# Kernel optimization log

Measured on AMD Instinct MI355X. Metric: run time of the kernel, lower is better.

The kernel has to match this reference:

```python
import jax, jax.numpy as jnp
import numpy as np

TOP_K = 2

def setup_inputs() -> dict:
    key = jax.random.key(0)
    k1, k2, k3, k4 = jax.random.split(key, 4)
    B, S, H, E, F = 2, 1024, 1024, 16, 1024
    hidden_states = jax.random.normal(k1, (B, S, H), dtype=jnp.float32)
    router_w = jax.random.normal(k2, (H, E), dtype=jnp.float32) * 0.02
    w_gate_up = jax.random.normal(k3, (E, H, 2 * F), dtype=jnp.float32) * 0.02
    w_down = jax.random.normal(k4, (E, F, H), dtype=jnp.float32) * 0.02
    return {"hidden_states": hidden_states, "router_w": router_w,
            "w_gate_up": w_gate_up, "w_down": w_down}

def reference(hidden_states, router_w, w_gate_up, w_down):
    B, S, H = hidden_states.shape
    E = router_w.shape[-1]
    flat = hidden_states.reshape(-1, H)                      # [T, H]
    T = flat.shape[0]
    # Routing: topk_then_softmax (default softmax_order)
    logits = flat @ router_w                                 # [T, E]
    top_vals, top_idx = jax.lax.top_k(logits, TOP_K)         # [T, K]
    routing_weights = jax.nn.softmax(top_vals, axis=-1)      # [T, K]
    # Scatter routing weights into a dense combine matrix [T, E]
    combine = jnp.zeros((T, E), dtype=flat.dtype)
    combine = combine.at[jnp.arange(T)[:, None], top_idx].add(routing_weights)
    # Fused expert FFN (per _FusedExpertTemplate, act_fn = SiLU-gated)
    gu = jnp.einsum('th,ehf->etf', flat, w_gate_up)          # [E, T, 2F]
    gate, up = jnp.split(gu, 2, axis=-1)
    gated = jax.nn.silu(gate) * up                           # [E, T, F]
    expert_out = jnp.einsum('etf,efh->eth', gated, w_down)   # [E, T, H]
    out = jnp.einsum('eth,te->th', expert_out, combine)      # [T, H]
    return out.reshape(B, S, H)
```

## Files before the change

kernel.cpp:

```cpp
#include <hip/hip_runtime.h>

#define T_TOK 2048
#define H_DIM 1024
#define E_NUM 16
#define F_DIM 1024
#define PNL 256

typedef unsigned short u16;
typedef unsigned int u32;
typedef short s16x8 __attribute__((ext_vector_type(8)));
typedef float f32x4 __attribute__((ext_vector_type(4)));

__device__ __forceinline__ float b2f(u16 v) { return __uint_as_float(((u32)v) << 16); }
__device__ __forceinline__ u16 f2b(float f) {
  u32 u = __float_as_uint(f);
  return (u16)((u + 0x7fffu + ((u >> 16) & 1u)) >> 16);
}

#define BARRIER()                                            \
  do {                                                       \
    asm volatile("s_waitcnt lgkmcnt(0)" ::: "memory");       \
    __builtin_amdgcn_sched_barrier(0);                       \
    __builtin_amdgcn_s_barrier();                            \
    __builtin_amdgcn_sched_barrier(0);                       \
  } while (0)

__global__ __launch_bounds__(256) void rw_transpose_kernel(const float* __restrict__ rw,
                                                           float* __restrict__ rwT) {
  int idx = blockIdx.x * 256 + threadIdx.x;
  float v = rw[idx];
  rwT[(idx & 15) * 1024 + (idx >> 4)] = v;
}

__global__ __launch_bounds__(256) void router_kernel(const float* __restrict__ hidden,
                                                     const float* __restrict__ rwT,
                                                     int* __restrict__ counts,
                                                     int* __restrict__ routing_e,
                                                     float* __restrict__ routing_w) {
  int wv = threadIdx.x >> 6, lane = threadIdx.x & 63;
  int t = blockIdx.x * 4 + wv;
  const float* xrow = hidden + (size_t)t * H_DIM;
  float acc[E_NUM];
#pragma unroll
  for (int e = 0; e < E_NUM; ++e) acc[e] = 0.f;
  for (int j = 0; j < H_DIM / 64; ++j) {
    int h = j * 64 + lane;
    float x = xrow[h];
#pragma unroll
    for (int e = 0; e < E_NUM; ++e) acc[e] += x * rwT[e * 1024 + h];
  }
#pragma unroll
  for (int e = 0; e < E_NUM; ++e) {
    acc[e] += __shfl_xor(acc[e], 32, 64);
    acc[e] += __shfl_xor(acc[e], 16, 64);
    acc[e] += __shfl_xor(acc[e], 8, 64);
    acc[e] += __shfl_xor(acc[e], 4, 64);
    acc[e] += __shfl_xor(acc[e], 2, 64);
    acc[e] += __shfl_xor(acc[e], 1, 64);
  }
  if (lane == 0) {
    float v0 = -1e30f, v1 = -1e30f;
    int i0 = 0, i1 = 0;
#pragma unroll
    for (int e = 0; e < E_NUM; ++e) {
      float v = acc[e];
      if (v > v0) { v1 = v0; i1 = i0; v0 = v; i0 = e; }
      else if (v > v1) { v1 = v; i1 = e; }
    }
    float p0 = 1.f / (1.f + __expf(v1 - v0));
    routing_e[2 * t] = i0;
    routing_e[2 * t + 1] = i1;
    routing_w[2 * t] = p0;
    routing_w[2 * t + 1] = 1.f - p0;
    atomicAdd(&counts[i0], 1);
    atomicAdd(&counts[i1], 1);
  }
}

__global__ void scatter_kernel(const int* __restrict__ counts, int* __restrict__ offsets,
                               const int* __restrict__ routing_e, const float* __restrict__ routing_w,
                               int* __restrict__ token_of_slot, float* __restrict__ slot_w) {
  __shared__ int offs[E_NUM];
  __shared__ int cur[E_NUM];
  int tid = threadIdx.x;
  if (tid == 0) {
    int s = 0;
    for (int e = 0; e < E_NUM; ++e) { offs[e] = s; s += counts[e]; }
  }
  __syncthreads();
  if (tid < E_NUM) { offsets[tid] = offs[tid]; cur[tid] = offs[tid]; }
  __syncthreads();
  for (int i = tid; i < 2 * T_TOK; i += 256) {
    int e = routing_e[i];
    int pos = atomicAdd(&cur[e], 1);
    token_of_slot[pos] = i >> 1;
    slot_w[pos] = routing_w[i];
  }
}

__device__ __forceinline__ void split_pack(const float* __restrict__ p, uint4& hh, uint4& ll) {
  u16 h[8], l[8];
#pragma unroll
  for (int i = 0; i < 8; ++i) {
    h[i] = f2b(p[i]);
    l[i] = f2b(p[i] - b2f(h[i]));
  }
  hh.x = (u32)h[0] | ((u32)h[1] << 16);
  hh.y = (u32)h[2] | ((u32)h[3] << 16);
  hh.z = (u32)h[4] | ((u32)h[5] << 16);
  hh.w = (u32)h[6] | ((u32)h[7] << 16);
  ll.x = (u32)l[0] | ((u32)l[1] << 16);
  ll.y = (u32)l[2] | ((u32)l[3] << 16);
  ll.z = (u32)l[4] | ((u32)l[5] << 16);
  ll.w = (u32)l[6] | ((u32)l[7] << 16);
}

__global__ __launch_bounds__(256) void prep_x(const float* __restrict__ x, u16* __restrict__ xh,
                                              u16* __restrict__ xl) {
  int i = blockIdx.x * 256 + threadIdx.x;
  float4 a = ((const float4*)x)[2 * i];
  float4 b = ((const float4*)x)[2 * i + 1];
  float v[8] = {a.x, a.y, a.z, a.w, b.x, b.y, b.z, b.w};
  uint4 hh, ll;
  split_pack(v, hh, ll);
  ((uint4*)xh)[i] = hh;
  ((uint4*)xl)[i] = ll;
}

__device__ __forceinline__ s16x8 read_bfrag(const u32* __restrict__ B, int n, int q) {
  return *(const s16x8*)&B[n * 16 + (((q ^ (n >> 3) ^ n) & 3) << 2)];
}

#define MFMA(a, b, c) __builtin_amdgcn_mfma_f32_16x16x32_bf16(a, b, c, 0, 0, 0)


#define WLOAD1(P, KK)                                              \
  {                                                                \
    const float* wp_ = wptr + (size_t)(KK) * 65536;                \
    P##0 = wp_[0];     P##1 = wp_[2048];  P##2 = wp_[4096];        \
    P##3 = wp_[6144];  P##4 = wp_[8192];  P##5 = wp_[10240];       \
    P##6 = wp_[12288]; P##7 = wp_[14336];                          \
  }

#define WCVT1(P, WW)                                               \
  {                                                                \
    WW.x = (u32)f2b(P##0) | ((u32)f2b(P##1) << 16);                \
    WW.y = (u32)f2b(P##2) | ((u32)f2b(P##3) << 16);                \
    WW.z = (u32)f2b(P##4) | ((u32)f2b(P##5) << 16);                \
    WW.w = (u32)f2b(P##6) | ((u32)f2b(P##7) << 16);                \
  }

__global__ __launch_bounds__(512, 2) void moe_gemm1(
    const u16* __restrict__ Xh, const u16* __restrict__ Xl, const float* __restrict__ wgu,
    const int* __restrict__ token_of_slot, const int* __restrict__ counts,
    const int* __restrict__ offsets, u16* __restrict__ act_h, u16* __restrict__ act_l) {
  const int e = blockIdx.y;
  const int cnt = counts[e];
  if (cnt == 0) return;
  const int off = offsets[e];
  const int f0 = blockIdx.x * 64;

  __shared__ u32 Bt[2][2048];

  const int tid = threadIdx.x;
  const int lane = tid & 63;
  const int wv = tid >> 6;
  const int q = lane >> 4, ln = lane & 15;
  const int mb = wv * 32;

  const int mat = tid >> 8;
  const int wn = ((tid >> 6) & 1) * 32 + ((tid & 63) >> 1);
  const int wh = ((tid >> 7) & 1) * 2 + (tid & 1);
  const float* wptr = wgu + (size_t)e * 2097152 + (size_t)(wh * 8) * 2048 + mat * 1024 + f0 + wn;
  const int wofs = mat * 1024 + wn * 16 + (((wh ^ (wn >> 3) ^ wn) & 3) << 2);

  float wa0, wa1, wa2, wa3, wa4, wa5, wa6, wa7;
  float wb0, wb1, wb2, wb3, wb4, wb5, wb6, wb7;
  s16x8 pH0, pH1, pL0, pL1, qH0, qH1, qL0, qL1;

#define G1IT(KK, PAR, WC, WN, H0, H1, L0, L1, NH0, NH1, NL0, NL1, NOTLAST, DOW) \
  {                                                                             \
    if (NOTLAST) {                                                              \
      const int ko_ = ((KK) + 1) * 32;                                          \
      NH0 = *(const s16x8*)(xh0 + ko_);                                         \
      NH1 = *(const s16x8*)(xh1 + ko_);                                         \
      NL0 = *(const s16x8*)(xl0 + ko_);                                         \
      NL1 = *(const s16x8*)(xl1 + ko_);                                         \
    }                                                                           \
    {                                                                           \
      const u32* Bc_ = &Bt[PAR][0];                                             \
      __builtin_amdgcn_s_setprio(1);                                            \
      _Pragma("unroll") for (int nf = 0; nf < 4; ++nf) {                        \
        s16x8 bg = read_bfrag(Bc_, nf * 16 + ln, q);                            \
        s16x8 bu = read_bfrag(Bc_ + 1024, nf * 16 + ln, q);                     \
        accg[0][nf] = MFMA(H0, bg, accg[0][nf]);                                \
        accg[1][nf] = MFMA(H1, bg, accg[1][nf]);                                \
        accg[0][nf] = MFMA(L0, bg, accg[0][nf]);                                \
        accg[1][nf] = MFMA(L1, bg, accg[1][nf]);                                \
        accu[0][nf] = MFMA(H0, bu, accu[0][nf]);                                \
        accu[1][nf] = MFMA(H1, bu, accu[1][nf]);                                \
        accu[0][nf] = MFMA(L0, bu, accu[0][nf]);                                \
        accu[1][nf] = MFMA(L1, bu, accu[1][nf]);                                \
      }                                                                         \
      __builtin_amdgcn_s_setprio(0);                                            \
    }                                                                           \
    if (NOTLAST) {                                                              \
      uint4 ww_;                                                                \
      WCVT1(WC, ww_);                                                           \
      *(uint4*)&Bt[1 - (PAR)][wofs] = ww_;                                      \
      if (DOW) WLOAD1(WN, (KK) + 2);                                            \
      BARRIER();                                                                \
    }                                                                           \
  }

  for (int p0 = 0; p0 < cnt; p0 += PNL) {
    const int rr0 = p0 + mb + ln, rr1 = rr0 + 16;
    const int t0 = (rr0 < cnt) ? token_of_slot[off + rr0] : 0;
    const int t1 = (rr1 < cnt) ? token_of_slot[off + rr1] : 0;
    const u16* xh0 = Xh + (size_t)t0 * H_DIM + q * 8;
    const u16* xh1 = Xh + (size_t)t1 * H_DIM + q * 8;
    const u16* xl0 = Xl + (size_t)t0 * H_DIM + q * 8;
    const u16* xl1 = Xl + (size_t)t1 * H_DIM + q * 8;

    f32x4 zero = {0.f, 0.f, 0.f, 0.f};
    f32x4 accg[2][4], accu[2][4];
#pragma unroll
    for (int i = 0; i < 2; ++i)
#pragma unroll
      for (int j = 0; j < 4; ++j) { accg[i][j] = zero; accu[i][j] = zero; }

    WLOAD1(wa, 0);
    pH0 = *(const s16x8*)(xh0);
    pH1 = *(const s16x8*)(xh1);
    pL0 = *(const s16x8*)(xl0);
    pL1 = *(const s16x8*)(xl1);
    {
      uint4 w0_;
      WCVT1(wa, w0_);
      *(uint4*)&Bt[0][wofs] = w0_;
    }
    WLOAD1(wb, 1);
    BARRIER();

    for (int kk = 0; kk < 28; kk += 2) {
      G1IT(kk, 0, wb, wa, pH0, pH1, pL0, pL1, qH0, qH1, qL0, qL1, 1, 1);
      G1IT(kk + 1, 1, wa, wb, qH0, qH1, qL0, qL1, pH0, pH1, pL0, pL1, 1, 1);
    }
    G1IT(28, 0, wb, wa, pH0, pH1, pL0, pL1, qH0, qH1, qL0, qL1, 1, 1);
    G1IT(29, 1, wa, wb, qH0, qH1, qL0, qL1, pH0, pH1, pL0, pL1, 1, 1);
    G1IT(30, 0, wb, wa, pH0, pH1, pL0, pL1, qH0, qH1, qL0, qL1, 1, 0);
    G1IT(31, 1, wa, wb, qH0, qH1, qL0, qL1, pH0, pH1, pL0, pL1, 0, 0);

#pragma unroll
    for (int m = 0; m < 2; ++m) {
#pragma unroll
      for (int r = 0; r < 4; ++r) {
        int rl = mb + m * 16 + q * 4 + r;
        int sr = p0 + rl;
        if (sr < cnt) {
          size_t rb = (size_t)(off + sr) * F_DIM + f0 + ln;
#pragma unroll
          for (int nf = 0; nf < 4; ++nf) {
            float g = accg[m][nf][r], u = accu[m][nf][r];
            float a = g * (1.f / (1.f + __expf(-g))) * u;
            u16 hh = f2b(a);
            act_h[rb + nf * 16] = hh;
            act_l[rb + nf * 16] = f2b(a - b2f(hh));
          }
        }
      }
    }
  }
}


#define WLOAD2(P, KK)                                       \
  {                                                         \
    const float* wp_ = wptr2 + (size_t)(KK) * 32768;        \
    P##0 = wp_[0];    P##1 = wp_[1024];                     \
    P##2 = wp_[2048]; P##3 = wp_[3072];                     \
  }

#define WCVT2(P, WW)                                        \
  {                                                         \
    WW.x = (u32)f2b(P##0) | ((u32)f2b(P##1) << 16);         \
    WW.y = (u32)f2b(P##2) | ((u32)f2b(P##3) << 16);         \
  }

__global__ __launch_bounds__(512, 2) void moe_gemm2(
    const u16* __restrict__ Ah, const u16* __restrict__ Al, const float* __restrict__ wd,
    const int* __restrict__ token_of_slot, const float* __restrict__ slot_w,
    const int* __restrict__ counts, const int* __restrict__ offsets,
    float* __restrict__ out) {
  const int e = blockIdx.y;
  const int cnt = counts[e];
  if (cnt == 0) return;
  const int off = offsets[e];
  const int h0 = blockIdx.x * 64;

  __shared__ u32 Bt[2][1024];

  const int tid = threadIdx.x;
  const int lane = tid & 63;
  const int wv = tid >> 6;
  const int q = lane >> 4, ln = lane & 15;
  const int mb = wv * 32;

  const int n2 = tid & 63, kpb = tid >> 6;
  const float* wptr2 = wd + (size_t)e * 1048576 + (size_t)(kpb * 4) * 1024 + h0 + n2;
  const int wofs2 = n2 * 16 + ((((kpb >> 1) ^ (n2 >> 3) ^ n2) & 3) << 2) + (kpb & 1) * 2;

  float wa0, wa1, wa2, wa3;
  float wb0, wb1, wb2, wb3;
  s16x8 pH0, pH1, pL0, pL1, qH0, qH1, qL0, qL1;

#define G2IT(KK, PAR, WC, WN, H0, H1, L0, L1, NH0, NH1, NL0, NL1, NOTLAST, DOW) \
  {                                                                             \
    if (NOTLAST) {                                                              \
      const int ko_ = ((KK) + 1) * 32;                                          \
      NH0 = *(const s16x8*)(ah0 + ko_);                                         \
      NH1 = *(const s16x8*)(ah1 + ko_);                                         \
      NL0 = *(const s16x8*)(al0 + ko_);                                         \
      NL1 = *(const s16x8*)(al1 + ko_);                                         \
    }                                                                           \
    {                                                                           \
      const u32* Bc_ = &Bt[PAR][0];                                             \
      __builtin_amdgcn_s_setprio(1);                                            \
      _Pragma("unroll") for (int nf = 0; nf < 4; ++nf) {                        \
        s16x8 bf = read_bfrag(Bc_, nf * 16 + ln, q);                            \
        acc[0][nf] = MFMA(H0, bf, acc[0][nf]);                                  \
        acc[1][nf] = MFMA(H1, bf, acc[1][nf]);                                  \
        acc[0][nf] = MFMA(L0, bf, acc[0][nf]);                                  \
        acc[1][nf] = MFMA(L1, bf, acc[1][nf]);                                  \
      }                                                                         \
      __builtin_amdgcn_s_setprio(0);                                            \
    }                                                                           \
    if (NOTLAST) {                                                              \
      uint2 ww_;                                                                \
      WCVT2(WC, ww_);                                                           \
      *(uint2*)&Bt[1 - (PAR)][wofs2] = ww_;                                     \
      if (DOW) WLOAD2(WN, (KK) + 2);                                            \
      BARRIER();                                                                \
    }                                                                           \
  }

  for (int p0 = 0; p0 < cnt; p0 += PNL) {
    const int rr0 = p0 + mb + ln, rr1 = rr0 + 16;
    const int s0 = off + ((rr0 < cnt) ? rr0 : 0);
    const int s1 = off + ((rr1 < cnt) ? rr1 : 0);
    const u16* ah0 = Ah + (size_t)s0 * F_DIM + q * 8;
    const u16* ah1 = Ah + (size_t)s1 * F_DIM + q * 8;
    const u16* al0 = Al + (size_t)s0 * F_DIM + q * 8;
    const u16* al1 = Al + (size_t)s1 * F_DIM + q * 8;

    f32x4 zero = {0.f, 0.f, 0.f, 0.f};
    f32x4 acc[2][4];
#pragma unroll
    for (int i = 0; i < 2; ++i)
#pragma unroll
      for (int j = 0; j < 4; ++j) acc[i][j] = zero;

    WLOAD2(wa, 0);
    pH0 = *(const s16x8*)(ah0);
    pH1 = *(const s16x8*)(ah1);
    pL0 = *(const s16x8*)(al0);
    pL1 = *(const s16x8*)(al1);
    {
      uint2 w0_;
      WCVT2(wa, w0_);
      *(uint2*)&Bt[0][wofs2] = w0_;
    }
    WLOAD2(wb, 1);
    BARRIER();

    for (int kk = 0; kk < 28; kk += 2) {
      G2IT(kk, 0, wb, wa, pH0, pH1, pL0, pL1, qH0, qH1, qL0, qL1, 1, 1);
      G2IT(kk + 1, 1, wa, wb, qH0, qH1, qL0, qL1, pH0, pH1, pL0, pL1, 1, 1);
    }
    G2IT(28, 0, wb, wa, pH0, pH1, pL0, pL1, qH0, qH1, qL0, qL1, 1, 1);
    G2IT(29, 1, wa, wb, qH0, qH1, qL0, qL1, pH0, pH1, pL0, pL1, 1, 1);
    G2IT(30, 0, wb, wa, pH0, pH1, pL0, pL1, qH0, qH1, qL0, qL1, 1, 0);
    G2IT(31, 1, wa, wb, qH0, qH1, qL0, qL1, pH0, pH1, pL0, pL1, 0, 0);

#pragma unroll
    for (int m = 0; m < 2; ++m) {
#pragma unroll
      for (int r = 0; r < 4; ++r) {
        int rl = mb + m * 16 + q * 4 + r;
        int sr = p0 + rl;
        if (sr < cnt) {
          int slot = off + sr;
          int tok = token_of_slot[slot];
          float wgt = slot_w[slot];
          float* orow = out + (size_t)tok * H_DIM + h0 + ln;
#pragma unroll
          for (int nf = 0; nf < 4; ++nf) atomicAdd(&orow[nf * 16], wgt * acc[m][nf][r]);
        }
      }
    }
  }
}

extern "C" void kernel_launch(void* const* d_in, const int* in_sizes, int n_in,
                              void* d_out, int out_size, void* d_ws, size_t ws_size,
                              hipStream_t stream) {
  const float* hidden = (const float*)d_in[0];
  const float* rw = (const float*)d_in[1];
  const float* wgu = (const float*)d_in[2];
  const float* wd = (const float*)d_in[3];
  float* out = (float*)d_out;
  char* ws = (char*)d_ws;

  int* counts = (int*)(ws);
  int* offsets = (int*)(ws + 256);
  int* routing_e = (int*)(ws + 1024);
  float* routing_w = (float*)(ws + 17408);
  int* token_of_slot = (int*)(ws + 33792);
  float* slot_w = (float*)(ws + 50176);
  float* rwT = (float*)(ws + 65536);
  u16* Xh = (u16*)(ws + 131072ull);
  u16* Xl = (u16*)(ws + 4325376ull);
  u16* act_h = (u16*)(ws + 8519680ull);
  u16* act_l = (u16*)(ws + 16908288ull);

  hipMemsetAsync(counts, 0, 64, stream);
  hipMemsetAsync(out, 0, (size_t)out_size * sizeof(float), stream);
  rw_transpose_kernel<<<dim3(64), dim3(256), 0, stream>>>(rw, rwT);
  router_kernel<<<dim3(T_TOK / 4), dim3(256), 0, stream>>>(hidden, rwT, counts, routing_e,
                                                           routing_w);
  scatter_kernel<<<dim3(1), dim3(256), 0, stream>>>(counts, offsets, routing_e, routing_w,
                                                    token_of_slot, slot_w);
  prep_x<<<dim3(T_TOK * H_DIM / 8 / 256), dim3(256), 0, stream>>>(hidden, Xh, Xl);
  moe_gemm1<<<dim3(16, 16), dim3(512), 0, stream>>>(Xh, Xl, wgu, token_of_slot, counts,
                                                    offsets, act_h, act_l);
  moe_gemm2<<<dim3(16, 16), dim3(512), 0, stream>>>(act_h, act_l, wd, token_of_slot,
                                                    slot_w, counts, offsets, out);
}
```

Measured before the change: 425.6 us.

## Flatten expert token panels into grid blocks with smaller 128-row panels

The scatter kernel now builds a flat list of (expert, panel-start) work items with 128-row panels. Both expert GEMM kernels launch one block per panel instead of one block per expert looping over its panels, with 16 rows per wave and a higher occupancy hint. The aim is to spread unevenly routed experts across more blocks and CUs, fixing load imbalance and underuse of the device. In exchange, each weight tile is reused across fewer rows and is reloaded and reconverted by more blocks, and per-wave MFMA work per barrier is halved.

```diff
diff --git a/kernel.cpp b/kernel.cpp
--- a/kernel.cpp
+++ b/kernel.cpp
@@ -4,7 +4,8 @@
 #define H_DIM 1024
 #define E_NUM 16
 #define F_DIM 1024
-#define PNL 256
+#define PNL 128
+#define MAXPAN 64
 
 typedef unsigned short u16;
 typedef unsigned int u32;
@@ -79,13 +80,19 @@
 
 __global__ void scatter_kernel(const int* __restrict__ counts, int* __restrict__ offsets,
                                const int* __restrict__ routing_e, const float* __restrict__ routing_w,
-                               int* __restrict__ token_of_slot, float* __restrict__ slot_w) {
+                               int* __restrict__ token_of_slot, float* __restrict__ slot_w,
+                               int* __restrict__ panel_e, int* __restrict__ panel_s,
+                               int* __restrict__ npan) {
   __shared__ int offs[E_NUM];
   __shared__ int cur[E_NUM];
   int tid = threadIdx.x;
   if (tid == 0) {
     int s = 0;
     for (int e = 0; e < E_NUM; ++e) { offs[e] = s; s += counts[e]; }
+    int np = 0;
+    for (int e = 0; e < E_NUM; ++e)
+      for (int p = 0; p < counts[e]; p += PNL) { panel_e[np] = e; panel_s[np] = p; ++np; }
+    *npan = np;
   }
   __syncthreads();
   if (tid < E_NUM) { offsets[tid] = offs[tid]; cur[tid] = offs[tid]; }
@@ -150,13 +157,17 @@
     WW.w = (u32)f2b(P##6) | ((u32)f2b(P##7) << 16);                \
   }
 
-__global__ __launch_bounds__(512, 2) void moe_gemm1(
+__global__ __launch_bounds__(512, 4) void moe_gemm1(
     const u16* __restrict__ Xh, const u16* __restrict__ Xl, const float* __restrict__ wgu,
     const int* __restrict__ token_of_slot, const int* __restrict__ counts,
-    const int* __restrict__ offsets, u16* __restrict__ act_h, u16* __restrict__ act_l) {
-  const int e = blockIdx.y;
+    const int* __restrict__ offsets, const int* __restrict__ panel_e,
+    const int* __restrict__ panel_s, const int* __restrict__ npan,
+    u16* __restrict__ act_h, u16* __restrict__ act_l) {
+  const int pid = blockIdx.y;
+  if (pid >= *npan) return;
+  const int e = panel_e[pid];
+  const int p0 = panel_s[pid];
   const int cnt = counts[e];
-  if (cnt == 0) return;
   const int off = offsets[e];
   const int f0 = blockIdx.x * 64;
 
@@ -166,7 +177,7 @@
   const int lane = tid & 63;
   const int wv = tid >> 6;
   const int q = lane >> 4, ln = lane & 15;
-  const int mb = wv * 32;
+  const int mb = wv * 16;
 
   const int mat = tid >> 8;
   const int wn = ((tid >> 6) & 1) * 32 + ((tid & 63) >> 1);
@@ -174,100 +185,82 @@
   const float* wptr = wgu + (size_t)e * 2097152 + (size_t)(wh * 8) * 2048 + mat * 1024 + f0 + wn;
   const int wofs = mat * 1024 + wn * 16 + (((wh ^ (wn >> 3) ^ wn) & 3) << 2);
 
+  const int rr0 = p0 + mb + ln;
+  const int t0 = (rr0 < cnt) ? token_of_slot[off + rr0] : 0;
+  const u16* xh0 = Xh + (size_t)t0 * H_DIM + q * 8;
+  const u16* xl0 = Xl + (size_t)t0 * H_DIM + q * 8;
+
   float wa0, wa1, wa2, wa3, wa4, wa5, wa6, wa7;
   float wb0, wb1, wb2, wb3, wb4, wb5, wb6, wb7;
-  s16x8 pH0, pH1, pL0, pL1, qH0, qH1, qL0, qL1;
-
-#define G1IT(KK, PAR, WC, WN, H0, H1, L0, L1, NH0, NH1, NL0, NL1, NOTLAST, DOW) \
-  {                                                                             \
-    if (NOTLAST) {                                                              \
-      const int ko_ = ((KK) + 1) * 32;                                          \
-      NH0 = *(const s16x8*)(xh0 + ko_);                                         \
-      NH1 = *(const s16x8*)(xh1 + ko_);                                         \
-      NL0 = *(const s16x8*)(xl0 + ko_);                                         \
-      NL1 = *(const s16x8*)(xl1 + ko_);                                         \
-    }                                                                           \
-    {                                                                           \
-      const u32* Bc_ = &Bt[PAR][0];                                             \
-      __builtin_amdgcn_s_setprio(1);                                            \
-      _Pragma("unroll") for (int nf = 0; nf < 4; ++nf) {                        \
-        s16x8 bg = read_bfrag(Bc_, nf * 16 + ln, q);                            \
-        s16x8 bu = read_bfrag(Bc_ + 1024, nf * 16 + ln, q);                     \
-        accg[0][nf] = MFMA(H0, bg, accg[0][nf]);                                \
-        accg[1][nf] = MFMA(H1, bg, accg[1][nf]);                                \
-        accg[0][nf] = MFMA(L0, bg, accg[0][nf]);                                \
-        accg[1][nf] = MFMA(L1, bg, accg[1][nf]);                                \
-        accu[0][nf] = MFMA(H0, bu, accu[0][nf]);                                \
-        accu[1][nf] = MFMA(H1, bu, accu[1][nf]);                                \
-        accu[0][nf] = MFMA(L0, bu, accu[0][nf]);                                \
-        accu[1][nf] = MFMA(L1, bu, accu[1][nf]);                                \
-      }                                                                         \
-      __builtin_amdgcn_s_setprio(0);                                            \
-    }                                                                           \
-    if (NOTLAST) {                                                              \
-      uint4 ww_;                                                                \
-      WCVT1(WC, ww_);                                                           \
-      *(uint4*)&Bt[1 - (PAR)][wofs] = ww_;                                      \
-      if (DOW) WLOAD1(WN, (KK) + 2);                                            \
-      BARRIER();                                                                \
-    }                                                                           \
-  }
-
-  for (int p0 = 0; p0 < cnt; p0 += PNL) {
-    const int rr0 = p0 + mb + ln, rr1 = rr0 + 16;
-    const int t0 = (rr0 < cnt) ? token_of_slot[off + rr0] : 0;
-    const int t1 = (rr1 < cnt) ? token_of_slot[off + rr1] : 0;
-    const u16* xh0 = Xh + (size_t)t0 * H_DIM + q * 8;
-    const u16* xh1 = Xh + (size_t)t1 * H_DIM + q * 8;
-    const u16* xl0 = Xl + (size_t)t0 * H_DIM + q * 8;
-    const u16* xl1 = Xl + (size_t)t1 * H_DIM + q * 8;
-
-    f32x4 zero = {0.f, 0.f, 0.f, 0.f};
-    f32x4 accg[2][4], accu[2][4];
-#pragma unroll
-    for (int i = 0; i < 2; ++i)
-#pragma unroll
-      for (int j = 0; j < 4; ++j) { accg[i][j] = zero; accu[i][j] = zero; }
-
-    WLOAD1(wa, 0);
-    pH0 = *(const s16x8*)(xh0);
-    pH1 = *(const s16x8*)(xh1);
-    pL0 = *(const s16x8*)(xl0);
-    pL1 = *(const s16x8*)(xl1);
-    {
-      uint4 w0_;
-      WCVT1(wa, w0_);
-      *(uint4*)&Bt[0][wofs] = w0_;
-    }
-    WLOAD1(wb, 1);
-    BARRIER();
-
-    for (int kk = 0; kk < 28; kk += 2) {
-      G1IT(kk, 0, wb, wa, pH0, pH1, pL0, pL1, qH0, qH1, qL0, qL1, 1, 1);
-      G1IT(kk + 1, 1, wa, wb, qH0, qH1, qL0, qL1, pH0, pH1, pL0, pL1, 1, 1);
-    }
-    G1IT(28, 0, wb, wa, pH0, pH1, pL0, pL1, qH0, qH1, qL0, qL1, 1, 1);
-    G1IT(29, 1, wa, wb, qH0, qH1, qL0, qL1, pH0, pH1, pL0, pL1, 1, 1);
-    G1IT(30, 0, wb, wa, pH0, pH1, pL0, pL1, qH0, qH1, qL0, qL1, 1, 0);
-    G1IT(31, 1, wa, wb, qH0, qH1, qL0, qL1, pH0, pH1, pL0, pL1, 0, 0);
-
-#pragma unroll
-    for (int m = 0; m < 2; ++m) {
-#pragma unroll
-      for (int r = 0; r < 4; ++r) {
-        int rl = mb + m * 16 + q * 4 + r;
-        int sr = p0 + rl;
-        if (sr < cnt) {
-          size_t rb = (size_t)(off + sr) * F_DIM + f0 + ln;
-#pragma unroll
-          for (int nf = 0; nf < 4; ++nf) {
-            float g = accg[m][nf][r], u = accu[m][nf][r];
-            float a = g * (1.f / (1.f + __expf(-g))) * u;
-            u16 hh = f2b(a);
-            act_h[rb + nf * 16] = hh;
-            act_l[rb + nf * 16] = f2b(a - b2f(hh));
-          }
-        }
+  s16x8 pH0, pL0, qH0, qL0;
+
+  f32x4 zero = {0.f, 0.f, 0.f, 0.f};
+  f32x4 accg[4], accu[4];
+#pragma unroll
+  for (int j = 0; j < 4; ++j) { accg[j] = zero; accu[j] = zero; }
+
+#define G1IT(KK, PAR, WC, WN, H0, L0, NH0, NL0, NOTLAST, DOW)    \
+  {                                                              \
+    if (NOTLAST) {                                               \
+      const int ko_ = ((KK) + 1) * 32;                           \
+      NH0 = *(const s16x8*)(xh0 + ko_);                          \
+      NL0 = *(const s16x8*)(xl0 + ko_);                          \
+    }                                                            \
+    {                                                            \
+      const u32* Bc_ = &Bt[PAR][0];                              \
+      __builtin_amdgcn_s_setprio(1);                             \
+      _Pragma("unroll") for (int nf = 0; nf < 4; ++nf) {         \
+        s16x8 bg = read_bfrag(Bc_, nf * 16 + ln, q);             \
+        s16x8 bu = read_bfrag(Bc_ + 1024, nf * 16 + ln, q);      \
+        accg[nf] = MFMA(H0, bg, accg[nf]);                       \
+        accg[nf] = MFMA(L0, bg, accg[nf]);                       \
+        accu[nf] = MFMA(H0, bu, accu[nf]);                       \
+        accu[nf] = MFMA(L0, bu, accu[nf]);                       \
+      }                                                          \
+      __builtin_amdgcn_s_setprio(0);                             \
+    }                                                            \
+    if (NOTLAST) {                                               \
+      uint4 ww_;                                                 \
+      WCVT1(WC, ww_);                                            \
+      *(uint4*)&Bt[1 - (PAR)][wofs] = ww_;                       \
+      if (DOW) WLOAD1(WN, (KK) + 2);                             \
+      BARRIER();                                                 \
+    }                                                            \
+  }
+
+  WLOAD1(wa, 0);
+  pH0 = *(const s16x8*)(xh0);
+  pL0 = *(const s16x8*)(xl0);
+  {
+    uint4 w0_;
+    WCVT1(wa, w0_);
+    *(uint4*)&Bt[0][wofs] = w0_;
+  }
+  WLOAD1(wb, 1);
+  BARRIER();
+
+  for (int kk = 0; kk < 28; kk += 2) {
+    G1IT(kk, 0, wb, wa, pH0, pL0, qH0, qL0, 1, 1);
+    G1IT(kk + 1, 1, wa, wb, qH0, qL0, pH0, pL0, 1, 1);
+  }
+  G1IT(28, 0, wb, wa, pH0, pL0, qH0, qL0, 1, 1);
+  G1IT(29, 1, wa, wb, qH0, qL0, pH0, pL0, 1, 1);
+  G1IT(30, 0, wb, wa, pH0, pL0, qH0, qL0, 1, 0);
+  G1IT(31, 1, wa, wb, qH0, qL0, pH0, pL0, 0, 0);
+
+#pragma unroll
+  for (int r = 0; r < 4; ++r) {
+    int rl = mb + q * 4 + r;
+    int sr = p0 + rl;
+    if (sr < cnt) {
+      size_t rb = (size_t)(off + sr) * F_DIM + f0 + ln;
+#pragma unroll
+      for (int nf = 0; nf < 4; ++nf) {
+        float g = accg[nf][r], u = accu[nf][r];
+        float a = g * (1.f / (1.f + __expf(-g))) * u;
+        u16 hh = f2b(a);
+        act_h[rb + nf * 16] = hh;
+        act_l[rb + nf * 16] = f2b(a - b2f(hh));
       }
     }
   }
@@ -287,14 +280,17 @@
     WW.y = (u32)f2b(P##2) | ((u32)f2b(P##3) << 16);         \
   }
 
-__global__ __launch_bounds__(512, 2) void moe_gemm2(
+__global__ __launch_bounds__(512, 4) void moe_gemm2(
     const u16* __restrict__ Ah, const u16* __restrict__ Al, const float* __restrict__ wd,
     const int* __restrict__ token_of_slot, const float* __restrict__ slot_w,
     const int* __restrict__ counts, const int* __restrict__ offsets,
-    float* __restrict__ out) {
-  const int e = blockIdx.y;
+    const int* __restrict__ panel_e, const int* __restrict__ panel_s,
+    const int* __restrict__ npan, float* __restrict__ out) {
+  const int pid = blockIdx.y;
+  if (pid >= *npan) return;
+  const int e = panel_e[pid];
+  const int p0 = panel_s[pid];
   const int cnt = counts[e];
-  if (cnt == 0) return;
   const int off = offsets[e];
   const int h0 = blockIdx.x * 64;
 
@@ -304,99 +300,83 @@
   const int lane = tid & 63;
   const int wv = tid >> 6;
   const int q = lane >> 4, ln = lane & 15;
-  const int mb = wv * 32;
+  const int mb = wv * 16;
 
   const int n2 = tid & 63, kpb = tid >> 6;
   const float* wptr2 = wd + (size_t)e * 1048576 + (size_t)(kpb * 4) * 1024 + h0 + n2;
   const int wofs2 = n2 * 16 + ((((kpb >> 1) ^ (n2 >> 3) ^ n2) & 3) << 2) + (kpb & 1) * 2;
 
+  const int rr0 = p0 + mb + ln;
+  const int s0 = off + ((rr0 < cnt) ? rr0 : 0);
+  const u16* ah0 = Ah + (size_t)s0 * F_DIM + q * 8;
+  const u16* al0 = Al + (size_t)s0 * F_DIM + q * 8;
+
   float wa0, wa1, wa2, wa3;
   float wb0, wb1, wb2, wb3;
-  s16x8 pH0, pH1, pL0, pL1, qH0, qH1, qL0, qL1;
-
-#define G2IT(KK, PAR, WC, WN, H0, H1, L0, L1, NH0, NH1, NL0, NL1, NOTLAST, DOW) \
-  {                                                                             \
-    if (NOTLAST) {                                                              \
-      const int ko_ = ((KK) + 1) * 32;                                          \
-      NH0 = *(const s16x8*)(ah0 + ko_);                                         \
-      NH1 = *(const s16x8*)(ah1 + ko_);                                         \
-      NL0 = *(const s16x8*)(al0 + ko_);                                         \
-      NL1 = *(const s16x8*)(al1 + ko_);                                         \
-    }                                                                           \
-    {                                                                           \
-      const u32* Bc_ = &Bt[PAR][0];                                             \
-      __builtin_amdgcn_s_setprio(1);                                            \
-      _Pragma("unroll") for (int nf = 0; nf < 4; ++nf) {                        \
-        s16x8 bf = read_bfrag(Bc_, nf * 16 + ln, q);                            \
-        acc[0][nf] = MFMA(H0, bf, acc[0][nf]);                                  \
-        acc[1][nf] = MFMA(H1, bf, acc[1][nf]);                                  \
-        acc[0][nf] = MFMA(L0, bf, acc[0][nf]);                                  \
-        acc[1][nf] = MFMA(L1, bf, acc[1][nf]);                                  \
-      }                                                                         \
-      __builtin_amdgcn_s_setprio(0);                                            \
-    }                                                                           \
-    if (NOTLAST) {                                                              \
-      uint2 ww_;                                                                \
-      WCVT2(WC, ww_);                                                           \
-      *(uint2*)&Bt[1 - (PAR)][wofs2] = ww_;                                     \
-      if (DOW) WLOAD2(WN, (KK) + 2);                                            \
-      BARRIER();                                                                \
-    }                                                                           \
-  }
-
-  for (int p0 = 0; p0 < cnt; p0 += PNL) {
-    const int rr0 = p0 + mb + ln, rr1 = rr0 + 16;
-    const int s0 = off + ((rr0 < cnt) ? rr0 : 0);
-    const int s1 = off + ((rr1 < cnt) ? rr1 : 0);
-    const u16* ah0 = Ah + (size_t)s0 * F_DIM + q * 8;
-    const u16* ah1 = Ah + (size_t)s1 * F_DIM + q * 8;
-    const u16* al0 = Al + (size_t)s0 * F_DIM + q * 8;
-    const u16* al1 = Al + (size_t)s1 * F_DIM + q * 8;
-
-    f32x4 zero = {0.f, 0.f, 0.f, 0.f};
-    f32x4 acc[2][4];
-#pragma unroll
-    for (int i = 0; i < 2; ++i)
-#pragma unroll
-      for (int j = 0; j < 4; ++j) acc[i][j] = zero;
-
-    WLOAD2(wa, 0);
-    pH0 = *(const s16x8*)(ah0);
-    pH1 = *(const s16x8*)(ah1);
-    pL0 = *(const s16x8*)(al0);
-    pL1 = *(const s16x8*)(al1);
-    {
-      uint2 w0_;
-      WCVT2(wa, w0_);
-      *(uint2*)&Bt[0][wofs2] = w0_;
-    }
-    WLOAD2(wb, 1);
-    BARRIER();
-
-    for (int kk = 0; kk < 28; kk += 2) {
-      G2IT(kk, 0, wb, wa, pH0, pH1, pL0, pL1, qH0, qH1, qL0, qL1, 1, 1);
-      G2IT(kk + 1, 1, wa, wb, qH0, qH1, qL0, qL1, pH0, pH1, pL0, pL1, 1, 1);
-    }
-    G2IT(28, 0, wb, wa, pH0, pH1, pL0, pL1, qH0, qH1, qL0, qL1, 1, 1);
-    G2IT(29, 1, wa, wb, qH0, qH1, qL0, qL1, pH0, pH1, pL0, pL1, 1, 1);
-    G2IT(30, 0, wb, wa, pH0, pH1, pL0, pL1, qH0, qH1, qL0, qL1, 1, 0);
-    G2IT(31, 1, wa, wb, qH0, qH1, qL0, qL1, pH0, pH1, pL0, pL1, 0, 0);
-
-#pragma unroll
-    for (int m = 0; m < 2; ++m) {
-#pragma unroll
-      for (int r = 0; r < 4; ++r) {
-        int rl = mb + m * 16 + q * 4 + r;
-        int sr = p0 + rl;
-        if (sr < cnt) {
-          int slot = off + sr;
-          int tok = token_of_slot[slot];
-          float wgt = slot_w[slot];
-          float* orow = out + (size_t)tok * H_DIM + h0 + ln;
-#pragma unroll
-          for (int nf = 0; nf < 4; ++nf) atomicAdd(&orow[nf * 16], wgt * acc[m][nf][r]);
-        }
-      }
+  s16x8 pH0, pL0, qH0, qL0;
+
+  f32x4 zero = {0.f, 0.f, 0.f, 0.f};
+  f32x4 acc[4];
+#pragma unroll
+  for (int j = 0; j < 4; ++j) acc[j] = zero;
+
+#define G2IT(KK, PAR, WC, WN, H0, L0, NH0, NL0, NOTLAST, DOW)    \
+  {                                                              \
+    if (NOTLAST) {                                               \
+      const int ko_ = ((KK) + 1) * 32;                           \
+      NH0 = *(const s16x8*)(ah0 + ko_);                          \
+      NL0 = *(const s16x8*)(al0 + ko_);                          \
+    }                                                            \
+    {                                                            \
+      const u32* Bc_ = &Bt[PAR][0];                              \
+      __builtin_amdgcn_s_setprio(1);                             \
+      _Pragma("unroll") for (int nf = 0; nf < 4; ++nf) {         \
+        s16x8 bf = read_bfrag(Bc_, nf * 16 + ln, q);             \
+        acc[nf] = MFMA(H0, bf, acc[nf]);                         \
+        acc[nf] = MFMA(L0, bf, acc[nf]);                         \
+      }                                                          \
+      __builtin_amdgcn_s_setprio(0);                             \
+    }                                                            \
+    if (NOTLAST) {                                               \
+      uint2 ww_;                                                 \
+      WCVT2(WC, ww_);                                            \
+      *(uint2*)&Bt[1 - (PAR)][wofs2] = ww_;                      \
+      if (DOW) WLOAD2(WN, (KK) + 2);                             \
+      BARRIER();                                                 \
+    }                                                            \
+  }
+
+  WLOAD2(wa, 0);
+  pH0 = *(const s16x8*)(ah0);
+  pL0 = *(const s16x8*)(al0);
+  {
+    uint2 w0_;
+    WCVT2(wa, w0_);
+    *(uint2*)&Bt[0][wofs2] = w0_;
+  }
+  WLOAD2(wb, 1);
+  BARRIER();
+
+  for (int kk = 0; kk < 28; kk += 2) {
+    G2IT(kk, 0, wb, wa, pH0, pL0, qH0, qL0, 1, 1);
+    G2IT(kk + 1, 1, wa, wb, qH0, qL0, pH0, pL0, 1, 1);
+  }
+  G2IT(28, 0, wb, wa, pH0, pL0, qH0, qL0, 1, 1);
+  G2IT(29, 1, wa, wb, qH0, qL0, pH0, pL0, 1, 1);
+  G2IT(30, 0, wb, wa, pH0, pL0, qH0, qL0, 1, 0);
+  G2IT(31, 1, wa, wb, qH0, qL0, pH0, pL0, 0, 0);
+
+#pragma unroll
+  for (int r = 0; r < 4; ++r) {
+    int rl = mb + q * 4 + r;
+    int sr = p0 + rl;
+    if (sr < cnt) {
+      int slot = off + sr;
+      int tok = token_of_slot[slot];
+      float wgt = slot_w[slot];
+      float* orow = out + (size_t)tok * H_DIM + h0 + ln;
+#pragma unroll
+      for (int nf = 0; nf < 4; ++nf) atomicAdd(&orow[nf * 16], wgt * acc[nf][r]);
     }
   }
 }
@@ -417,11 +397,14 @@
   float* routing_w = (float*)(ws + 17408);
   int* token_of_slot = (int*)(ws + 33792);
   float* slot_w = (float*)(ws + 50176);
-  float* rwT = (float*)(ws + 65536);
-  u16* Xh = (u16*)(ws + 131072ull);
-  u16* Xl = (u16*)(ws + 4325376ull);
-  u16* act_h = (u16*)(ws + 8519680ull);
-  u16* act_l = (u16*)(ws + 16908288ull);
+  int* panel_e = (int*)(ws + 66560);
+  int* panel_s = (int*)(ws + 66816);
+  int* npan = (int*)(ws + 67072);
+  float* rwT = (float*)(ws + 69632);
+  u16* Xh = (u16*)(ws + 262144ull);
+  u16* Xl = (u16*)(ws + 4456448ull);
+  u16* act_h = (u16*)(ws + 8650752ull);
+  u16* act_l = (u16*)(ws + 17039360ull);
 
   hipMemsetAsync(counts, 0, 64, stream);
   hipMemsetAsync(out, 0, (size_t)out_size * sizeof(float), stream);
@@ -429,10 +412,13 @@
   router_kernel<<<dim3(T_TOK / 4), dim3(256), 0, stream>>>(hidden, rwT, counts, routing_e,
                                                            routing_w);
   scatter_kernel<<<dim3(1), dim3(256), 0, stream>>>(counts, offsets, routing_e, routing_w,
-                                                    token_of_slot, slot_w);
+                                                    token_of_slot, slot_w, panel_e, panel_s,
+                                                    npan);
   prep_x<<<dim3(T_TOK * H_DIM / 8 / 256), dim3(256), 0, stream>>>(hidden, Xh, Xl);
-  moe_gemm1<<<dim3(16, 16), dim3(512), 0, stream>>>(Xh, Xl, wgu, token_of_slot, counts,
-                                                    offsets, act_h, act_l);
-  moe_gemm2<<<dim3(16, 16), dim3(512), 0, stream>>>(act_h, act_l, wd, token_of_slot,
-                                                    slot_w, counts, offsets, out);
-}
+  moe_gemm1<<<dim3(16, 48), dim3(512), 0, stream>>>(Xh, Xl, wgu, token_of_slot, counts,
+                                                    offsets, panel_e, panel_s, npan,
+                                                    act_h, act_l);
+  moe_gemm2<<<dim3(16, 48), dim3(512), 0, stream>>>(act_h, act_l, wd, token_of_slot, slot_w,
+                                                    counts, offsets, panel_e, panel_s, npan,
+                                                    out);
+}
```

Result: slower. 452.7 us (+6.4%).
